# Kernel optimization log

Measured on AMD Instinct MI355X. Metric: run time of the kernel, lower is better.

## Reference

```python
import jax, jax.numpy as jnp
import numpy as np

B, S, D, H, L, V = 32, 100, 1024, 16, 2, 32000
DF = 4 * D
EPS_LN = 1e-5
EPS_Q = 1e-6


def _ln(x, scale, bias):
    mu = jnp.mean(x, axis=-1, keepdims=True)
    var = jnp.mean(jnp.square(x - mu), axis=-1, keepdims=True)
    return (x - mu) * jax.lax.rsqrt(var + EPS_LN) * scale + bias


def setup_inputs() -> dict:
    key = jax.random.key(0)
    ks = jax.random.split(key, 20)
    sd = 0.02
    inp = {
        "x": jax.random.randint(ks[0], (B, S), 0, V),
        "emb": jax.random.normal(ks[1], (V, D), jnp.float32) * sd,
        "pos_emb": jax.random.normal(ks[2], (100, D), jnp.float32) * sd,
        "qkv_w": jax.random.normal(ks[3], (L, 3 * D, D), jnp.float32) * sd,
        "qkv_b": jnp.zeros((L, 3 * D), jnp.float32),
        "out_w": jax.random.normal(ks[4], (L, D, D), jnp.float32) * sd,
        "out_b": jnp.zeros((L, D), jnp.float32),
        "ln1_s": jnp.ones((L, D), jnp.float32),
        "ln1_b": jnp.zeros((L, D), jnp.float32),
        "ff1_w": jax.random.normal(ks[5], (L, DF, D), jnp.float32) * sd,
        "ff1_b": jnp.zeros((L, DF), jnp.float32),
        "ff2_w": jax.random.normal(ks[6], (L, D, DF), jnp.float32) * sd,
        "ff2_b": jnp.zeros((L, D), jnp.float32),
        "ln2_s": jnp.ones((L, D), jnp.float32),
        "ln2_b": jnp.zeros((L, D), jnp.float32),
        "dec_w": jax.random.normal(ks[7], (V, D), jnp.float32) * sd,
        "dec_b": jnp.zeros((V,), jnp.float32),
    }
    return inp


def reference(x, emb, pos_emb, qkv_w, qkv_b, out_w, out_b, ln1_s, ln1_b,
              ff1_w, ff1_b, ff2_w, ff2_b, ln2_s, ln2_b, dec_w, dec_b):
    hd = D // H
    h = emb[x] + pos_emb[:S][None, :, :]  # [B,S,D]
    for l in range(L):
        qkv = h @ qkv_w[l].T + qkv_b[l]  # [B,S,3D]
        q, k, v = jnp.split(qkv, 3, axis=-1)
        q = q.reshape(B, S, H, hd).transpose(0, 2, 1, 3)
        k = k.reshape(B, S, H, hd).transpose(0, 2, 1, 3)
        v = v.reshape(B, S, H, hd).transpose(0, 2, 1, 3)
        scores = jnp.einsum('bhqd,bhkd->bhqk', q, k) / jnp.sqrt(jnp.float32(hd))
        attn = jax.nn.softmax(scores, axis=-1)
        ctx = jnp.einsum('bhqk,bhkd->bhqd', attn, v)
        ctx = ctx.transpose(0, 2, 1, 3).reshape(B, S, D)
        attn_out = ctx @ out_w[l].T + out_b[l]
        h = _ln(h + attn_out, ln1_s[l], ln1_b[l])  # post-norm
        ff = jax.nn.gelu(h @ ff1_w[l].T + ff1_b[l], approximate=False) @ ff2_w[l].T + ff2_b[l]
        h = _ln(h + ff, ln2_s[l], ln2_b[l])
    # Ternary decoder (faithful to the original pack/unpack semantics:
    # packed code = q+1; unpack adds x when code==1 (q==0) and subtracts when
    # code==2 (q==+1), i.e. effective weight = {q==0: +1, q==+1: -1, q==-1: 0}).
    g = jnp.mean(jnp.abs(dec_w))
    wq = jnp.clip(jnp.round(dec_w / (g + EPS_Q)), -1.0, 1.0)
    w_eff = jnp.where(wq == 0.0, 1.0, jnp.where(wq == 1.0, -1.0, 0.0)).astype(jnp.float32)
    return h @ w_eff.T + dec_b  # [B,S,V]
```

## Files before the change

### kernel.cpp

```cpp
#include <hip/hip_runtime.h>
#include <hip/hip_bf16.h>
#include <math.h>

#define B_ 32
#define S_ 100
#define D_ 1024
#define H_ 16
#define L_ 2
#define V_ 32000
#define DF_ 4096
#define HD_ 64
#define MPAD 3328

typedef __bf16 bf16x8 __attribute__((ext_vector_type(8)));
typedef float f32x4 __attribute__((ext_vector_type(4)));

__device__ __forceinline__ void async_copy16(const void* g, void* l) {
  __builtin_amdgcn_global_load_lds((const __attribute__((address_space(1))) void*)g,
                                   (__attribute__((address_space(3))) void*)l, 16, 0, 0);
}

__global__ void absmean_kernel(const float* __restrict__ w, double* __restrict__ out) {
  const long long n4 = (long long)V_ * D_ / 4;
  double s = 0.0;
  long long stride = (long long)gridDim.x * blockDim.x;
  for (long long i = (long long)blockIdx.x * blockDim.x + threadIdx.x; i < n4; i += stride) {
    float4 v = ((const float4*)w)[i];
    s += (double)fabsf(v.x) + (double)fabsf(v.y) + (double)fabsf(v.z) + (double)fabsf(v.w);
  }
#pragma unroll
  for (int off = 32; off > 0; off >>= 1) s += __shfl_down(s, off);
  __shared__ double sm[4];
  int lane = threadIdx.x & 63, wv = threadIdx.x >> 6;
  if (lane == 0) sm[wv] = s;
  __syncthreads();
  if (threadIdx.x == 0) atomicAdd(out, sm[0] + sm[1] + sm[2] + sm[3]);
}

__global__ void quantize_kernel(const float* __restrict__ w, const double* __restrict__ gsum,
                                __hip_bfloat16* __restrict__ q) {
  const long long n4 = (long long)V_ * D_ / 4;
  double g = (*gsum) / ((double)V_ * D_) + 1e-6;
  long long stride = (long long)gridDim.x * blockDim.x;
  for (long long i = (long long)blockIdx.x * blockDim.x + threadIdx.x; i < n4; i += stride) {
    float4 v = ((const float4*)w)[i];
    union { __hip_bfloat16 h[4]; uint2 u; } o;
    float vv[4] = {v.x, v.y, v.z, v.w};
#pragma unroll
    for (int j = 0; j < 4; ++j) {
      double r = rint((double)vv[j] / g);
      r = fmin(1.0, fmax(-1.0, r));
      float w_eff = (r == 0.0) ? 1.0f : ((r == 1.0) ? -1.0f : 0.0f);
      o.h[j] = __float2bfloat16(w_eff);
    }
    ((uint2*)q)[i] = o.u;
  }
}

__global__ void cast_all_kernel(const float* __restrict__ qkv_w, const float* __restrict__ out_w,
                                const float* __restrict__ ff1_w, const float* __restrict__ ff2_w,
                                __hip_bfloat16* __restrict__ qd, __hip_bfloat16* __restrict__ od,
                                __hip_bfloat16* __restrict__ f1d, __hip_bfloat16* __restrict__ f2d) {
  const long long n1 = (long long)2 * 3072 * 1024 / 4;
  const long long n2 = n1 + (long long)2 * 1024 * 1024 / 4;
  const long long n3 = n2 + (long long)2 * 4096 * 1024 / 4;
  const long long n4 = n3 + (long long)2 * 1024 * 4096 / 4;
  long long stride = (long long)gridDim.x * blockDim.x;
  for (long long i = (long long)blockIdx.x * blockDim.x + threadIdx.x; i < n4; i += stride) {
    const float* src; __hip_bfloat16* dst; long long j;
    if (i < n1)      { src = qkv_w; dst = qd;  j = i; }
    else if (i < n2) { src = out_w; dst = od;  j = i - n1; }
    else if (i < n3) { src = ff1_w; dst = f1d; j = i - n2; }
    else             { src = ff2_w; dst = f2d; j = i - n3; }
    float4 v = ((const float4*)src)[j];
    union { __hip_bfloat16 h[4]; uint2 u; } o;
    o.h[0] = __float2bfloat16(v.x);
    o.h[1] = __float2bfloat16(v.y);
    o.h[2] = __float2bfloat16(v.z);
    o.h[3] = __float2bfloat16(v.w);
    ((uint2*)dst)[j] = o.u;
  }
}

__global__ __launch_bounds__(256) void embed_kernel(const int* __restrict__ x,
    const float* __restrict__ emb, const float* __restrict__ pos,
    float* __restrict__ h, __hip_bfloat16* __restrict__ hb) {
  int row = blockIdx.x;
  int s = row % S_;
  int tok = x[row];
  size_t eb = (size_t)tok * D_, pb = (size_t)s * D_, hb0 = (size_t)row * D_;
#pragma unroll
  for (int i = 0; i < 4; ++i) {
    int d = threadIdx.x + i * 256;
    float v = emb[eb + d] + pos[pb + d];
    h[hb0 + d] = v;
    hb[hb0 + d] = __float2bfloat16(v);
  }
}

__device__ __forceinline__ float gelu_exact(float v) {
  return 0.5f * v * (1.0f + erff(v * 0.70710678118654752f));
}

template <int ACT, int OUTBF>
__global__ __launch_bounds__(256) void gemm_bf(const __hip_bfloat16* __restrict__ A,
    const __hip_bfloat16* __restrict__ Bm, const float* __restrict__ bias,
    void* __restrict__ C, void* __restrict__ C2, int M, int N, int K, int lda, int ldb) {
  __shared__ __bf16 As[128 * 64];
  __shared__ __bf16 Bs[128 * 64];
  int tid = threadIdx.x;
  int lane = tid & 63, wid = tid >> 6;
  int wr = wid >> 1, wc = wid & 1;
  int z = blockIdx.z;

  int nwg = gridDim.x * gridDim.y;
  int orig = blockIdx.y * gridDim.x + blockIdx.x;
  int q = nwg >> 3, r = nwg & 7;
  int xcd = orig & 7, local = orig >> 3;
  int wgid = (xcd < r ? xcd * (q + 1) : r * (q + 1) + (xcd - r) * q) + local;
  int row0 = (wgid % gridDim.x) * 128;
  int col0 = (wgid / gridDim.x) * 128;

  const __hip_bfloat16* Az = A + (size_t)z * K;
  const __hip_bfloat16* Bz = Bm + (size_t)z * K;
  int j0 = wid * 2;
  const __hip_bfloat16* Ag0 = Az + (size_t)(row0 + j0 * 16 + (lane >> 2)) * lda + (lane & 3) * 8;
  const __hip_bfloat16* Ag1 = Az + (size_t)(row0 + (j0 + 1) * 16 + (lane >> 2)) * lda + (lane & 3) * 8;
  const __hip_bfloat16* Bg0 = Bz + (size_t)(col0 + j0 * 16 + (lane >> 2)) * ldb + (lane & 3) * 8;
  const __hip_bfloat16* Bg1 = Bz + (size_t)(col0 + (j0 + 1) * 16 + (lane >> 2)) * ldb + (lane & 3) * 8;
  __bf16* Al0 = As + j0 * 512;
  __bf16* Al1 = As + (j0 + 1) * 512;
  __bf16* Bl0 = Bs + j0 * 512;
  __bf16* Bl1 = Bs + (j0 + 1) * 512;

  float bias_v[4];
#pragma unroll
  for (int ni = 0; ni < 4; ++ni)
    bias_v[ni] = (z == 0) ? bias[col0 + wc * 64 + ni * 16 + (lane & 15)] : 0.f;

  f32x4 acc[4][4];
#pragma unroll
  for (int mi = 0; mi < 4; ++mi)
#pragma unroll
    for (int ni = 0; ni < 4; ++ni) acc[mi][ni] = (f32x4){0.f, 0.f, 0.f, 0.f};

  const bf16x8* Asv = reinterpret_cast<const bf16x8*>(As);
  const bf16x8* Bsv = reinterpret_cast<const bf16x8*>(Bs);
  int afr = (wr * 64 + (lane & 15)) * 4 + (lane >> 4);
  int bfr = (wc * 64 + (lane & 15)) * 4 + (lane >> 4);

  for (int k0 = 0; k0 < K; k0 += 64) {
    async_copy16(Ag0, Al0);  async_copy16(Ag0 + 32, (char*)Al0 + 8192);
    async_copy16(Ag1, Al1);  async_copy16(Ag1 + 32, (char*)Al1 + 8192);
    async_copy16(Bg0, Bl0);  async_copy16(Bg0 + 32, (char*)Bl0 + 8192);
    async_copy16(Bg1, Bl1);  async_copy16(Bg1 + 32, (char*)Bl1 + 8192);
    Ag0 += 64; Ag1 += 64; Bg0 += 64; Bg1 += 64;
    __syncthreads();
    bf16x8 af[4][2], bq[4][2];
#pragma unroll
    for (int mi = 0; mi < 4; ++mi)
#pragma unroll
      for (int kk = 0; kk < 2; ++kk) af[mi][kk] = Asv[afr + mi * 64 + kk * 512];
#pragma unroll
    for (int ni = 0; ni < 4; ++ni)
#pragma unroll
      for (int kk = 0; kk < 2; ++kk) bq[ni][kk] = Bsv[bfr + ni * 64 + kk * 512];
#pragma unroll
    for (int mi = 0; mi < 4; ++mi)
#pragma unroll
      for (int ni = 0; ni < 4; ++ni)
#pragma unroll
        for (int kk = 0; kk < 2; ++kk)
          acc[mi][ni] = __builtin_amdgcn_mfma_f32_16x16x32_bf16(af[mi][kk], bq[ni][kk], acc[mi][ni], 0, 0, 0);
    __syncthreads();
  }

  float* Cf = (float*)((z == 0) ? C : C2);
  __hip_bfloat16* Cb = (__hip_bfloat16*)C;
#pragma unroll
  for (int mi = 0; mi < 4; ++mi) {
#pragma unroll
    for (int r2 = 0; r2 < 4; ++r2) {
      size_t m = row0 + wr * 64 + mi * 16 + (lane >> 4) * 4 + r2;
#pragma unroll
      for (int ni = 0; ni < 4; ++ni) {
        size_t n = col0 + wc * 64 + ni * 16 + (lane & 15);
        float v = acc[mi][ni][r2] + bias_v[ni];
        if (ACT == 1) v = gelu_exact(v);
        if (OUTBF) Cb[m * N + n] = __float2bfloat16(v);
        else       Cf[m * N + n] = v;
      }
    }
  }
}

__global__ __launch_bounds__(512, 1) void gemm256_dec(
    const __hip_bfloat16* __restrict__ A, const __hip_bfloat16* __restrict__ Bm,
    const float* __restrict__ bias, float* __restrict__ C,
    int Mreal, int N, int K) {
  extern __shared__ char lds[];
  char* ldsA = lds;
  char* ldsB = lds + 65536;
  const int t = threadIdx.x;
  const int lane = t & 63, wid = t >> 6;
  const int wm = wid >> 2, wn = wid & 3;
  const int NT = K >> 6;

  int nwg = gridDim.x * gridDim.y;
  int orig = blockIdx.y * gridDim.x + blockIdx.x;
  int q = nwg >> 3, r = nwg & 7;
  int xcd = orig & 7, local = orig >> 3;
  int wgid = (xcd < r ? xcd * (q + 1) : r * (q + 1) + (xcd - r) * q) + local;
  int row0 = (wgid % gridDim.x) * 256;
  int col0 = (wgid / gridDim.x) * 256;

  const int rs = t >> 2;
  const int kc = ((((t & 3) << 4) ^ (((t >> 5) & 1) << 5)) >> 1);
  const __hip_bfloat16* Asrc = A + (size_t)(row0 + rs) * K + kc;
  const __hip_bfloat16* Bsrc = Bm + (size_t)(col0 + rs) * K + kc;

#define STAGE_A(b, h, tgt) do { \
    const __hip_bfloat16* _s = Asrc + (size_t)(h) * 128 * K + (tgt) * 64; \
    char* _d = ldsA + (b) * 32768 + (h) * 16384 + t * 16; \
    async_copy16(_s, _d); async_copy16(_s + 32, _d + 8192); } while (0)
#define STAGE_B(b, h, tgt) do { \
    const __hip_bfloat16* _s = Bsrc + (size_t)(h) * 128 * K + (tgt) * 64; \
    char* _d = ldsB + (b) * 32768 + (h) * 16384 + t * 16; \
    async_copy16(_s, _d); async_copy16(_s + 32, _d + 8192); } while (0)
#define SB() __builtin_amdgcn_sched_barrier(0)
#define BAR() __builtin_amdgcn_s_barrier()

  const int sb5 = ((lane >> 3) & 1) << 5;
  const int laneoff = ((lane & 15) << 6) + (((lane >> 4) << 4) ^ sb5);

  f32x4 acc[8][4];
#pragma unroll
  for (int i = 0; i < 8; ++i)
#pragma unroll
    for (int j = 0; j < 4; ++j) acc[i][j] = (f32x4){0.f, 0.f, 0.f, 0.f};

  STAGE_A(0, 0, 0); STAGE_B(0, 0, 0); STAGE_A(0, 1, 0); STAGE_B(0, 1, 0);
  STAGE_B(1, 0, 1); STAGE_A(1, 0, 1);
  asm volatile("s_waitcnt vmcnt(4)" ::: "memory");
  SB(); BAR(); SB();

  bf16x8 a[4][2], b[4][2];
  for (int T = 0; T < NT; ++T) {
    const int bs = T & 1;
    const char* Aw = ldsA + bs * 32768 + wm * 16384 + laneoff;
    const char* Bw = ldsB + bs * 32768 + (wn >> 1) * 16384 + (wn & 1) * 4096 + laneoff;
#pragma unroll
    for (int mi = 0; mi < 4; ++mi)
#pragma unroll
      for (int kk = 0; kk < 2; ++kk)
        a[mi][kk] = *(const bf16x8*)(Aw + mi * 1024 + kk * 8192);
#pragma unroll
    for (int ni = 0; ni < 2; ++ni)
#pragma unroll
      for (int kk = 0; kk < 2; ++kk)
        b[ni][kk] = *(const bf16x8*)(Bw + ni * 1024 + kk * 8192);
    if (T + 1 < NT) STAGE_A(bs ^ 1, 1, T + 1);
    SB(); BAR(); SB();
    __builtin_amdgcn_s_setprio(1);
#pragma unroll
    for (int mi = 0; mi < 4; ++mi)
#pragma unroll
      for (int ni = 0; ni < 2; ++ni)
#pragma unroll
        for (int kk = 0; kk < 2; ++kk)
          acc[mi][ni] = __builtin_amdgcn_mfma_f32_16x16x32_bf16(a[mi][kk], b[ni][kk], acc[mi][ni], 0, 0, 0);
    __builtin_amdgcn_s_setprio(0);
    SB(); BAR(); SB();
#pragma unroll
    for (int ni = 2; ni < 4; ++ni)
#pragma unroll
      for (int kk = 0; kk < 2; ++kk)
        b[ni][kk] = *(const bf16x8*)(Bw + ni * 1024 + kk * 8192);
    if (T + 1 < NT) STAGE_B(bs ^ 1, 1, T + 1);
    SB(); BAR(); SB();
    __builtin_amdgcn_s_setprio(1);
#pragma unroll
    for (int mi = 0; mi < 4; ++mi)
#pragma unroll
      for (int ni = 2; ni < 4; ++ni)
#pragma unroll
        for (int kk = 0; kk < 2; ++kk)
          acc[mi][ni] = __builtin_amdgcn_mfma_f32_16x16x32_bf16(a[mi][kk], b[ni][kk], acc[mi][ni], 0, 0, 0);
    __builtin_amdgcn_s_setprio(0);
    SB(); BAR(); SB();
#pragma unroll
    for (int mi = 0; mi < 4; ++mi)
#pragma unroll
      for (int kk = 0; kk < 2; ++kk)
        a[mi][kk] = *(const bf16x8*)(Aw + (mi + 4) * 1024 + kk * 8192);
    if (T + 2 < NT) STAGE_B(bs, 0, T + 2);
    SB(); BAR(); SB();
    __builtin_amdgcn_s_setprio(1);
#pragma unroll
    for (int mi = 0; mi < 4; ++mi)
#pragma unroll
      for (int ni = 0; ni < 2; ++ni)
#pragma unroll
        for (int kk = 0; kk < 2; ++kk)
          acc[mi + 4][ni] = __builtin_amdgcn_mfma_f32_16x16x32_bf16(a[mi][kk], b[ni][kk], acc[mi + 4][ni], 0, 0, 0);
    __builtin_amdgcn_s_setprio(0);
    SB(); BAR(); SB();
    if (T + 2 < NT) STAGE_A(bs, 0, T + 2);
    if (T < NT - 2) { asm volatile("s_waitcnt vmcnt(4)" ::: "memory"); }
    else            { asm volatile("s_waitcnt vmcnt(0)" ::: "memory"); }
    SB(); BAR(); SB();
    __builtin_amdgcn_s_setprio(1);
#pragma unroll
    for (int mi = 0; mi < 4; ++mi)
#pragma unroll
      for (int ni = 2; ni < 4; ++ni)
#pragma unroll
        for (int kk = 0; kk < 2; ++kk)
          acc[mi + 4][ni] = __builtin_amdgcn_mfma_f32_16x16x32_bf16(a[mi][kk], b[ni][kk], acc[mi + 4][ni], 0, 0, 0);
    __builtin_amdgcn_s_setprio(0);
    SB(); BAR(); SB();
  }
#undef STAGE_A
#undef STAGE_B
#undef SB
#undef BAR

  float bias_v[4];
#pragma unroll
  for (int ni = 0; ni < 4; ++ni)
    bias_v[ni] = bias[col0 + wn * 64 + ni * 16 + (lane & 15)];
#pragma unroll
  for (int mi = 0; mi < 8; ++mi) {
#pragma unroll
    for (int r2 = 0; r2 < 4; ++r2) {
      int m = row0 + wm * 128 + mi * 16 + (lane >> 4) * 4 + r2;
      if (m < Mreal) {
#pragma unroll
        for (int ni = 0; ni < 4; ++ni) {
          int n = col0 + wn * 64 + ni * 16 + (lane & 15);
          C[(size_t)m * N + n] = acc[mi][ni][r2] + bias_v[ni];
        }
      }
    }
  }
}

__global__ __launch_bounds__(128) void attn_kernel(const __hip_bfloat16* __restrict__ qkv,
                                                   __hip_bfloat16* __restrict__ ctx) {
  __shared__ float KV[50][64];
  __shared__ float Sc[100][101];
  int bh = blockIdx.x;
  int b = bh >> 4, hh = bh & 15;
  int tid = threadIdx.x;
  size_t base = (size_t)b * S_ * (3 * D_);
  int hcol = hh * HD_;
  int r = tid;

  float qa[64];
  if (r < 100) {
    const __hip_bfloat16* qp = qkv + base + (size_t)r * (3 * D_) + hcol;
#pragma unroll
    for (int d0 = 0; d0 < 8; ++d0) {
      union { uint4 u; __hip_bfloat16 h[8]; } uu;
      uu.u = *(const uint4*)(qp + d0 * 8);
#pragma unroll
      for (int j = 0; j < 8; ++j) qa[d0 * 8 + j] = __bfloat162float(uu.h[j]);
    }
  }
  for (int tt = 0; tt < 2; ++tt) {
    __syncthreads();
    for (int idx = tid; idx < 400; idx += 128) {
      int j = idx >> 3, d8 = idx & 7;
      union { uint4 u; __hip_bfloat16 h[8]; } uu;
      uu.u = *(const uint4*)(qkv + base + (size_t)(tt * 50 + j) * (3 * D_) + D_ + hcol + d8 * 8);
#pragma unroll
      for (int e = 0; e < 8; ++e) KV[j][d8 * 8 + e] = __bfloat162float(uu.h[e]);
    }
    __syncthreads();
    if (r < 100) {
      for (int j = 0; j < 50; ++j) {
        float s = 0.f;
#pragma unroll
        for (int d0 = 0; d0 < 16; ++d0) {
          float4 kv = *(const float4*)&KV[j][d0 * 4];
          s += qa[d0 * 4 + 0] * kv.x + qa[d0 * 4 + 1] * kv.y +
               qa[d0 * 4 + 2] * kv.z + qa[d0 * 4 + 3] * kv.w;
        }
        Sc[r][tt * 50 + j] = s * 0.125f;
      }
    }
  }
  float inv_sum = 0.f;
  if (r < 100) {
    float mx = -1e30f;
    for (int j = 0; j < 100; ++j) mx = fmaxf(mx, Sc[r][j]);
    float sum = 0.f;
    for (int j = 0; j < 100; ++j) {
      float e = expf(Sc[r][j] - mx);
      Sc[r][j] = e;
      sum += e;
    }
    inv_sum = 1.0f / sum;
  }
  float ca[64];
#pragma unroll
  for (int d = 0; d < 64; ++d) ca[d] = 0.f;
  for (int tt = 0; tt < 2; ++tt) {
    __syncthreads();
    for (int idx = tid; idx < 400; idx += 128) {
      int j = idx >> 3, d8 = idx & 7;
      union { uint4 u; __hip_bfloat16 h[8]; } uu;
      uu.u = *(const uint4*)(qkv + base + (size_t)(tt * 50 + j) * (3 * D_) + 2 * D_ + hcol + d8 * 8);
#pragma unroll
      for (int e = 0; e < 8; ++e) KV[j][d8 * 8 + e] = __bfloat162float(uu.h[e]);
    }
    __syncthreads();
    if (r < 100) {
      for (int j = 0; j < 50; ++j) {
        float p = Sc[r][tt * 50 + j];
#pragma unroll
        for (int d0 = 0; d0 < 16; ++d0) {
          float4 kv = *(const float4*)&KV[j][d0 * 4];
          ca[d0 * 4 + 0] += p * kv.x;
          ca[d0 * 4 + 1] += p * kv.y;
          ca[d0 * 4 + 2] += p * kv.z;
          ca[d0 * 4 + 3] += p * kv.w;
        }
      }
    }
  }
  if (r < 100) {
    __hip_bfloat16* cp = ctx + ((size_t)b * S_ + r) * D_ + hcol;
#pragma unroll
    for (int d = 0; d < 64; ++d) cp[d] = __float2bfloat16(ca[d] * inv_sum);
  }
}

__device__ float block_sum_1024(float v) {
#pragma unroll
  for (int off = 32; off > 0; off >>= 1) v += __shfl_down(v, off);
  __shared__ float sm[4];
  __syncthreads();
  int lane = threadIdx.x & 63, wv = threadIdx.x >> 6;
  if (lane == 0) sm[wv] = v;
  __syncthreads();
  return sm[0] + sm[1] + sm[2] + sm[3];
}

__global__ __launch_bounds__(256) void add_ln_kernel(float* __restrict__ h,
    const float* __restrict__ res, const float* __restrict__ res2,
    const float* __restrict__ scale, const float* __restrict__ bias,
    __hip_bfloat16* __restrict__ hb) {
  size_t b4 = (size_t)blockIdx.x * 256 + threadIdx.x;
  float4 xa = ((const float4*)h)[b4];
  float4 xb = ((const float4*)res)[b4];
  float x[4] = {xa.x + xb.x, xa.y + xb.y, xa.z + xb.z, xa.w + xb.w};
  if (res2) {
    float4 xc = ((const float4*)res2)[b4];
    x[0] += xc.x; x[1] += xc.y; x[2] += xc.z; x[3] += xc.w;
  }
  float s = x[0] + x[1] + x[2] + x[3];
  float mu = block_sum_1024(s) * (1.0f / 1024.0f);
  float v = 0.f;
#pragma unroll
  for (int i = 0; i < 4; ++i) {
    float d = x[i] - mu;
    v += d * d;
  }
  float var = block_sum_1024(v) * (1.0f / 1024.0f);
  float rs = rsqrtf(var + 1e-5f);
  int d0 = threadIdx.x * 4;
  float4 sc = *(const float4*)&scale[d0];
  float4 bi = *(const float4*)&bias[d0];
  float o[4];
  o[0] = (x[0] - mu) * rs * sc.x + bi.x;
  o[1] = (x[1] - mu) * rs * sc.y + bi.y;
  o[2] = (x[2] - mu) * rs * sc.z + bi.z;
  o[3] = (x[3] - mu) * rs * sc.w + bi.w;
  ((float4*)h)[b4] = (float4){o[0], o[1], o[2], o[3]};
  union { __hip_bfloat16 hh[4]; uint2 u; } ob;
#pragma unroll
  for (int i = 0; i < 4; ++i) ob.hh[i] = __float2bfloat16(o[i]);
  ((uint2*)hb)[b4] = ob.u;
}

extern "C" void kernel_launch(void* const* d_in, const int* in_sizes, int n_in,
                              void* d_out, int out_size, void* d_ws, size_t ws_size,
                              hipStream_t stream) {
  const int* x       = (const int*)d_in[0];
  const float* emb   = (const float*)d_in[1];
  const float* pos   = (const float*)d_in[2];
  const float* qkv_w = (const float*)d_in[3];
  const float* qkv_b = (const float*)d_in[4];
  const float* out_w = (const float*)d_in[5];
  const float* out_b = (const float*)d_in[6];
  const float* ln1_s = (const float*)d_in[7];
  const float* ln1_b = (const float*)d_in[8];
  const float* ff1_w = (const float*)d_in[9];
  const float* ff1_b = (const float*)d_in[10];
  const float* ff2_w = (const float*)d_in[11];
  const float* ff2_b = (const float*)d_in[12];
  const float* ln2_s = (const float*)d_in[13];
  const float* ln2_b = (const float*)d_in[14];
  const float* dec_w = (const float*)d_in[15];
  const float* dec_b = (const float*)d_in[16];
  float* out = (float*)d_out;

  char* ws = (char*)d_ws;
  size_t off = 0;
  auto alloc = [&](size_t bytes) { void* p = ws + off; off += (bytes + 255) & ~(size_t)255; return p; };
  double* gsum            = (double*)alloc(256);
  float* h                = (float*)alloc((size_t)3200 * 1024 * 4);
  __hip_bfloat16* h_bf    = (__hip_bfloat16*)alloc((size_t)MPAD * 1024 * 2);
  float* tmp              = (float*)alloc((size_t)3200 * 1024 * 4);
  float* tmp2             = (float*)alloc((size_t)3200 * 1024 * 4);
  __hip_bfloat16* ctx_bf  = (__hip_bfloat16*)alloc((size_t)3200 * 1024 * 2);
  __hip_bfloat16* big_bf  = (__hip_bfloat16*)alloc((size_t)3200 * 4096 * 2);
  __hip_bfloat16* weff    = (__hip_bfloat16*)alloc((size_t)32000 * 1024 * 2);
  __hip_bfloat16* qkvw_bf = (__hip_bfloat16*)alloc((size_t)2 * 3072 * 1024 * 2);
  __hip_bfloat16* outw_bf = (__hip_bfloat16*)alloc((size_t)2 * 1024 * 1024 * 2);
  __hip_bfloat16* ff1w_bf = (__hip_bfloat16*)alloc((size_t)2 * 4096 * 1024 * 2);
  __hip_bfloat16* ff2w_bf = (__hip_bfloat16*)alloc((size_t)2 * 1024 * 4096 * 2);

  hipMemsetAsync(gsum, 0, 256, stream);
  absmean_kernel<<<2048, 256, 0, stream>>>(dec_w, gsum);
  quantize_kernel<<<4096, 256, 0, stream>>>(dec_w, gsum, weff);
  cast_all_kernel<<<4096, 256, 0, stream>>>(qkv_w, out_w, ff1_w, ff2_w,
                                            qkvw_bf, outw_bf, ff1w_bf, ff2w_bf);
  embed_kernel<<<3200, 256, 0, stream>>>(x, emb, pos, h, h_bf);

  const int M = 3200;
  for (int l = 0; l < 2; ++l) {
    gemm_bf<0, 1><<<dim3(M / 128, 3072 / 128, 1), 256, 0, stream>>>(
        h_bf, qkvw_bf + (size_t)l * 3072 * 1024, qkv_b + l * 3072, big_bf, nullptr,
        M, 3072, 1024, 1024, 1024);
    attn_kernel<<<512, 128, 0, stream>>>(big_bf, ctx_bf);
    gemm_bf<0, 0><<<dim3(M / 128, 1024 / 128, 2), 256, 0, stream>>>(
        ctx_bf, outw_bf + (size_t)l * 1024 * 1024, out_b + l * 1024, tmp, tmp2,
        M, 1024, 512, 1024, 1024);
    add_ln_kernel<<<M, 256, 0, stream>>>(h, tmp, tmp2, ln1_s + l * 1024, ln1_b + l * 1024, h_bf);
    gemm_bf<1, 1><<<dim3(M / 128, 4096 / 128, 1), 256, 0, stream>>>(
        h_bf, ff1w_bf + (size_t)l * 4096 * 1024, ff1_b + l * 4096, big_bf, nullptr,
        M, 4096, 1024, 1024, 1024);
    gemm_bf<0, 0><<<dim3(M / 128, 1024 / 128, 2), 256, 0, stream>>>(
        big_bf, ff2w_bf + (size_t)l * 1024 * 4096, ff2_b + l * 1024, tmp, tmp2,
        M, 1024, 2048, 4096, 4096);
    add_ln_kernel<<<M, 256, 0, stream>>>(h, tmp, tmp2, ln2_s + l * 1024, ln2_b + l * 1024, h_bf);
  }
  gemm256_dec<<<dim3(MPAD / 256, 32000 / 256), 512, 131072, stream>>>(
      h_bf, weff, dec_b, out, M, 32000, 1024);
}
```

Measured before the change: 924.9 us.

## Double-buffer LDS tiles in bf16 GEMM to overlap global loads with MFMA

The GEMM now keeps two LDS stages for the A and B tiles. While MFMAs run on the current stage, the async global-to-LDS copies for the next K-tile are issued into the other stage. A single waitcnt plus barrier per iteration replaces the two `__syncthreads` calls, which is meant to hide global memory latency behind compute. The cost is double the LDS per block (64KB), and launch bounds of 256 threads with 2 blocks per CU are set to keep occupancy.

```diff
diff --git a/kernel.cpp b/kernel.cpp
--- a/kernel.cpp
+++ b/kernel.cpp
@@ -103,11 +103,11 @@
 }
 
 template <int ACT, int OUTBF>
-__global__ __launch_bounds__(256) void gemm_bf(const __hip_bfloat16* __restrict__ A,
+__global__ __launch_bounds__(256, 2) void gemm_bf(const __hip_bfloat16* __restrict__ A,
     const __hip_bfloat16* __restrict__ Bm, const float* __restrict__ bias,
     void* __restrict__ C, void* __restrict__ C2, int M, int N, int K, int lda, int ldb) {
-  __shared__ __bf16 As[128 * 64];
-  __shared__ __bf16 Bs[128 * 64];
+  __shared__ __bf16 As[2 * 128 * 64];
+  __shared__ __bf16 Bs[2 * 128 * 64];
   int tid = threadIdx.x;
   int lane = tid & 63, wid = tid >> 6;
   int wr = wid >> 1, wc = wid & 1;
@@ -128,10 +128,22 @@
   const __hip_bfloat16* Ag1 = Az + (size_t)(row0 + (j0 + 1) * 16 + (lane >> 2)) * lda + (lane & 3) * 8;
   const __hip_bfloat16* Bg0 = Bz + (size_t)(col0 + j0 * 16 + (lane >> 2)) * ldb + (lane & 3) * 8;
   const __hip_bfloat16* Bg1 = Bz + (size_t)(col0 + (j0 + 1) * 16 + (lane >> 2)) * ldb + (lane & 3) * 8;
-  __bf16* Al0 = As + j0 * 512;
-  __bf16* Al1 = As + (j0 + 1) * 512;
-  __bf16* Bl0 = Bs + j0 * 512;
-  __bf16* Bl1 = Bs + (j0 + 1) * 512;
+  char* AsB = (char*)As;
+  char* BsB = (char*)Bs;
+
+#define STG(bf, tgt) do { \
+    const __hip_bfloat16* _a0 = Ag0 + (size_t)(tgt) * 64; \
+    const __hip_bfloat16* _a1 = Ag1 + (size_t)(tgt) * 64; \
+    const __hip_bfloat16* _b0 = Bg0 + (size_t)(tgt) * 64; \
+    const __hip_bfloat16* _b1 = Bg1 + (size_t)(tgt) * 64; \
+    char* _da = AsB + (bf) * 16384 + j0 * 1024; \
+    char* _db = BsB + (bf) * 16384 + j0 * 1024; \
+    async_copy16(_a0, _da);          async_copy16(_a0 + 32, _da + 8192); \
+    async_copy16(_a1, _da + 1024);   async_copy16(_a1 + 32, _da + 9216); \
+    async_copy16(_b0, _db);          async_copy16(_b0 + 32, _db + 8192); \
+    async_copy16(_b1, _db + 1024);   async_copy16(_b1 + 32, _db + 9216); } while (0)
+#define SB() __builtin_amdgcn_sched_barrier(0)
+#define BAR() __builtin_amdgcn_s_barrier()
 
   float bias_v[4];
 #pragma unroll
@@ -144,27 +156,28 @@
 #pragma unroll
     for (int ni = 0; ni < 4; ++ni) acc[mi][ni] = (f32x4){0.f, 0.f, 0.f, 0.f};
 
-  const bf16x8* Asv = reinterpret_cast<const bf16x8*>(As);
-  const bf16x8* Bsv = reinterpret_cast<const bf16x8*>(Bs);
-  int afr = (wr * 64 + (lane & 15)) * 4 + (lane >> 4);
-  int bfr = (wc * 64 + (lane & 15)) * 4 + (lane >> 4);
-
-  for (int k0 = 0; k0 < K; k0 += 64) {
-    async_copy16(Ag0, Al0);  async_copy16(Ag0 + 32, (char*)Al0 + 8192);
-    async_copy16(Ag1, Al1);  async_copy16(Ag1 + 32, (char*)Al1 + 8192);
-    async_copy16(Bg0, Bl0);  async_copy16(Bg0 + 32, (char*)Bl0 + 8192);
-    async_copy16(Bg1, Bl1);  async_copy16(Bg1 + 32, (char*)Bl1 + 8192);
-    Ag0 += 64; Ag1 += 64; Bg0 += 64; Bg1 += 64;
-    __syncthreads();
+  int afr = ((wr * 64 + (lane & 15)) * 4 + (lane >> 4)) * 16;
+  int bfr = ((wc * 64 + (lane & 15)) * 4 + (lane >> 4)) * 16;
+
+  const int NT = K >> 6;
+  STG(0, 0);
+  asm volatile("s_waitcnt vmcnt(0)" ::: "memory");
+  SB(); BAR(); SB();
+
+  for (int t = 0; t < NT; ++t) {
+    const int cur = t & 1;
+    if (t + 1 < NT) STG(cur ^ 1, t + 1);
+    const char* Aw = AsB + cur * 16384 + afr;
+    const char* Bw = BsB + cur * 16384 + bfr;
     bf16x8 af[4][2], bq[4][2];
 #pragma unroll
     for (int mi = 0; mi < 4; ++mi)
 #pragma unroll
-      for (int kk = 0; kk < 2; ++kk) af[mi][kk] = Asv[afr + mi * 64 + kk * 512];
+      for (int kk = 0; kk < 2; ++kk) af[mi][kk] = *(const bf16x8*)(Aw + mi * 1024 + kk * 8192);
 #pragma unroll
     for (int ni = 0; ni < 4; ++ni)
 #pragma unroll
-      for (int kk = 0; kk < 2; ++kk) bq[ni][kk] = Bsv[bfr + ni * 64 + kk * 512];
+      for (int kk = 0; kk < 2; ++kk) bq[ni][kk] = *(const bf16x8*)(Bw + ni * 1024 + kk * 8192);
 #pragma unroll
     for (int mi = 0; mi < 4; ++mi)
 #pragma unroll
@@ -172,8 +185,12 @@
 #pragma unroll
         for (int kk = 0; kk < 2; ++kk)
           acc[mi][ni] = __builtin_amdgcn_mfma_f32_16x16x32_bf16(af[mi][kk], bq[ni][kk], acc[mi][ni], 0, 0, 0);
-    __syncthreads();
-  }
+    asm volatile("s_waitcnt vmcnt(0)" ::: "memory");
+    SB(); BAR(); SB();
+  }
+#undef STG
+#undef SB
+#undef BAR
 
   float* Cf = (float*)((z == 0) ? C : C2);
   __hip_bfloat16* Cb = (__hip_bfloat16*)C;
```

Measured after the change: 940.0 us. Within noise of the previous version (+1.6%).
